# Performance work log

Hardware: AMD Instinct MI355X
Metric: run time of the kernel (lower is better)

The kernel has to match this reference:

```python
import jax, jax.numpy as jnp
import numpy as np

D = 512        # latent_dim
DT = 256       # text_latent_dim
H = 8          # num_heads
TE = 2048      # time_embed_dim
NEG = -1000000.0


def _ln(x, g, b, eps=1e-5):
    m = jnp.mean(x, axis=-1, keepdims=True)
    v = jnp.mean(jnp.square(x - m), axis=-1, keepdims=True)
    return (x - m) * jax.lax.rsqrt(v + eps) * g + b


def _linear(x, W, b):
    return x @ W.T + b


def setup_inputs() -> dict:
    key = jax.random.key(0)
    ks = jax.random.split(key, 24)
    B, T, NT, R, LR = 32, 1024, 77, 4, 256
    inp = {
        'x': jax.random.normal(ks[0], (B, T, D), jnp.float32),
        'xf': jax.random.normal(ks[1], (B, NT, DT), jnp.float32),
        'emb': jax.random.normal(ks[2], (B, TE), jnp.float32),
        'src_mask': jax.random.randint(ks[3], (B, T, 1), 0, 2).astype(jnp.float32),
        'cond_type': jax.random.randint(ks[4], (B, 1, 1), 0, 100).astype(jnp.int32),
        're_motion': jax.random.normal(ks[5], (B, R, LR, D), jnp.float32),
        're_text': jax.random.normal(ks[6], (B, R, 1, D), jnp.float32),
        're_mask': jax.random.randint(ks[7], (B, R, LR), 0, 2).astype(jnp.float32),
    }
    s = 0.02
    def W(k, o, i):
        return jax.random.normal(k, (o, i), jnp.float32) * s
    params = {
        'norm_g': jnp.ones((D,), jnp.float32), 'norm_b': jnp.zeros((D,), jnp.float32),
        'tnorm_g': jnp.ones((DT,), jnp.float32), 'tnorm_b': jnp.zeros((DT,), jnp.float32),
        'rn1_g': jnp.ones((2 * D,), jnp.float32), 'rn1_b': jnp.zeros((2 * D,), jnp.float32),
        'rn2_g': jnp.ones((D,), jnp.float32), 'rn2_b': jnp.zeros((D,), jnp.float32),
        'Wq': W(ks[8], D, D), 'bq': jnp.zeros((D,), jnp.float32),
        'Wkt': W(ks[9], D, DT), 'bkt': jnp.zeros((D,), jnp.float32),
        'Wvt': W(ks[10], D, DT), 'bvt': jnp.zeros((D,), jnp.float32),
        'Wkm': W(ks[11], D, D), 'bkm': jnp.zeros((D,), jnp.float32),
        'Wvm': W(ks[12], D, D), 'bvm': jnp.zeros((D,), jnp.float32),
        'Wkr': W(ks[13], D, 2 * D), 'bkr': jnp.zeros((D,), jnp.float32),
        'Wvr': W(ks[14], D, D), 'bvr': jnp.zeros((D,), jnp.float32),
        'emb_W': W(ks[15], 2 * D, TE), 'emb_b': jnp.zeros((2 * D,), jnp.float32),
        'snorm_g': jnp.ones((D,), jnp.float32), 'snorm_b': jnp.zeros((D,), jnp.float32),
        'out_W': W(ks[16], D, D), 'out_b': jnp.zeros((D,), jnp.float32),
    }
    inp.update(params)
    return inp


def _forward(x, xf, emb, src_mask, cond_type, re_motion, re_text, re_mask,
             norm_g, norm_b, tnorm_g, tnorm_b, rn1_g, rn1_b, rn2_g, rn2_b,
             Wq, bq, Wkt, bkt, Wvt, bvt, Wkm, bkm, Wvm, bvm, Wkr, bkr, Wvr, bvr,
             emb_W, emb_b, snorm_g, snorm_b, out_W, out_b):
    B, T, _ = x.shape
    re_mask_r = re_mask.reshape(B, -1, 1)                       # [B, R*LR, 1]
    N = xf.shape[1] + T + re_motion.shape[1] * re_motion.shape[2]

    xn = _ln(x, norm_g, norm_b)                                  # [B,T,D]
    xfn = _ln(xf, tnorm_g, tnorm_b)                              # [B,NT,DT]
    query = _linear(xn, Wq, bq)                                  # [B,T,D]

    text_ct = (cond_type % 10 > 0).astype(x.dtype)               # [B,1,1]
    retr_ct = (cond_type // 10 > 0).astype(x.dtype)              # [B,1,1]

    re_text_rep = jnp.broadcast_to(re_text, re_motion.shape)     # repeat along Lr
    re_feat_key = jnp.concatenate([re_motion, re_text_rep], axis=-1).reshape(B, -1, 2 * D)

    k_text = _linear(xfn, Wkt, bkt) + (1.0 - text_ct) * NEG
    k_retr = (_linear(_ln(re_feat_key, rn1_g, rn1_b), Wkr, bkr)
              + (1.0 - retr_ct) * NEG + (1.0 - re_mask_r) * NEG)
    k_mot = _linear(xn, Wkm, bkm) + (1.0 - src_mask) * NEG
    key_cat = jnp.concatenate([k_text, k_retr, k_mot], axis=1)   # [B,N,D]

    q = jax.nn.softmax(query.reshape(B, T, H, -1), axis=-1)      # softmax over head_dim
    k = jax.nn.softmax(key_cat.reshape(B, N, H, -1), axis=1)     # softmax over tokens

    re_feat_value = re_motion.reshape(B, -1, D)
    v_text = _linear(xfn, Wvt, bvt) * text_ct
    v_retr = _linear(_ln(re_feat_value, rn2_g, rn2_b), Wvr, bvr) * retr_ct * re_mask_r
    v_mot = _linear(xn, Wvm, bvm) * src_mask
    v = jnp.concatenate([v_text, v_retr, v_mot], axis=1).reshape(B, N, H, -1)

    attention = jnp.einsum('bnhd,bnhl->bhdl', k, v)              # [B,H,hd,hd]
    y = jnp.einsum('bthd,bhdl->bthl', q, attention).reshape(B, T, D)

    # StylizationBlock: film-style scale/shift from time embedding, zero-init out proj
    emb_out = _linear(jax.nn.silu(emb), emb_W, emb_b)[:, None, :]  # [B,1,2D]
    scale, shift = emb_out[..., :D], emb_out[..., D:]
    h = _ln(y, snorm_g, snorm_b) * (1.0 + scale) + shift
    h = _linear(jax.nn.silu(h), out_W, out_b)
    return x + h


def reference(x, xf, emb, src_mask, cond_type, re_motion, re_text, re_mask,
              norm_g, norm_b, tnorm_g, tnorm_b, rn1_g, rn1_b, rn2_g, rn2_b,
              Wq, bq, Wkt, bkt, Wvt, bvt, Wkm, bkm, Wvm, bvm, Wkr, bkr, Wvr, bvr,
              emb_W, emb_b, snorm_g, snorm_b, out_W, out_b):
    return _forward(x, xf, emb, src_mask, cond_type, re_motion, re_text, re_mask,
                    norm_g, norm_b, tnorm_g, tnorm_b, rn1_g, rn1_b, rn2_g, rn2_b,
                    Wq, bq, Wkt, bkt, Wvt, bvt, Wkm, bkm, Wvm, bvm, Wkr, bkr, Wvr, bvr,
                    emb_W, emb_b, snorm_g, snorm_b, out_W, out_b)
```

## Files before the change

kernel.cpp:

```cpp
#include <hip/hip_runtime.h>
#include <cstddef>
#include <cstdint>

#define DEV __device__ __forceinline__

namespace {

constexpr int kH = 8;
constexpr int kB = 32, kT = 1024, kNT = 77, kR = 4, kLR = 256;
constexpr int kRL = kR * kLR;
constexpr float kNEG = -1000000.0f;
constexpr int kNtot = 2304;
constexpr int kNS2 = 3;

typedef __bf16 bf16x8 __attribute__((ext_vector_type(8)));
typedef float f32x4 __attribute__((ext_vector_type(4)));

DEV unsigned short f2bf(float f) {
  unsigned int u = __float_as_uint(f);
  u += 0x7fffu + ((u >> 16) & 1u);
  return (unsigned short)(u >> 16);
}
DEV float bf2f(unsigned short h) { return __uint_as_float(((unsigned int)h) << 16); }

DEV float wave_sum(float v) {
  #pragma unroll
  for (int s = 32; s; s >>= 1) v += __shfl_xor(v, s);
  return v;
}

DEV int xcd_swz(int bid, int nwg) {
  if ((nwg & 7) == 0) return (bid & 7) * (nwg >> 3) + (bid >> 3);
  return bid;
}

template<int COLS>
__global__ __launch_bounds__(256) void ln_bf16(const float* __restrict__ in,
    const float* __restrict__ g, const float* __restrict__ be,
    unsigned short* __restrict__ out) {
  constexpr int PT = COLS / 256;
  int row = blockIdx.x;
  const float* p = in + (size_t)row * COLS;
  unsigned short* o = out + (size_t)row * COLS;
  float v[PT]; float s = 0.f, s2 = 0.f;
  #pragma unroll
  for (int i = 0; i < PT; i++) {
    v[i] = p[threadIdx.x + i * 256];
    s += v[i]; s2 += v[i] * v[i];
  }
  __shared__ float red[2][4];
  int lane = threadIdx.x & 63, w = threadIdx.x >> 6;
  s = wave_sum(s); s2 = wave_sum(s2);
  if (!lane) { red[0][w] = s; red[1][w] = s2; }
  __syncthreads();
  s = red[0][0] + red[0][1] + red[0][2] + red[0][3];
  s2 = red[1][0] + red[1][1] + red[1][2] + red[1][3];
  float mean = s / COLS;
  float var = s2 / COLS - mean * mean;
  float rstd = rsqrtf(var + 1e-5f);
  #pragma unroll
  for (int i = 0; i < PT; i++) {
    int c = threadIdx.x + i * 256;
    o[c] = f2bf((v[i] - mean) * rstd * g[c] + be[c]);
  }
}

__global__ __launch_bounds__(256) void rfk_stats(const float* __restrict__ mot,
    const float* __restrict__ txt, unsigned short* __restrict__ mot_bf,
    float* __restrict__ s1k, float* __restrict__ s2k,
    float* __restrict__ s1v, float* __restrict__ s2v) {
  int m = blockIdx.x;
  const float* pm = mot + (size_t)m * 512;
  const float* pt = txt + (size_t)(m >> 8) * 512;
  float v[2], t[2];
  float sv = 0.f, sv2 = 0.f, st = 0.f, st2 = 0.f;
  #pragma unroll
  for (int i = 0; i < 2; i++) {
    v[i] = pm[threadIdx.x + i * 256]; sv += v[i]; sv2 += v[i] * v[i];
    t[i] = pt[threadIdx.x + i * 256]; st += t[i]; st2 += t[i] * t[i];
  }
  __shared__ float red[4][4];
  int lane = threadIdx.x & 63, w = threadIdx.x >> 6;
  sv = wave_sum(sv); sv2 = wave_sum(sv2); st = wave_sum(st); st2 = wave_sum(st2);
  if (!lane) { red[0][w] = sv; red[1][w] = sv2; red[2][w] = st; red[3][w] = st2; }
  __syncthreads();
  #pragma unroll
  for (int i = 0; i < 2; i++)
    mot_bf[(size_t)m * 512 + threadIdx.x + i * 256] = f2bf(v[i]);
  if (threadIdx.x == 0) {
    float SV = red[0][0] + red[0][1] + red[0][2] + red[0][3];
    float SV2 = red[1][0] + red[1][1] + red[1][2] + red[1][3];
    float ST = red[2][0] + red[2][1] + red[2][2] + red[2][3];
    float ST2 = red[3][0] + red[3][1] + red[3][2] + red[3][3];
    float SA = SV + ST, SA2 = SV2 + ST2;
    float ma = SA / 1024.f, va = SA2 / 1024.f - ma * ma;
    float ra = rsqrtf(va + 1e-5f);
    float mv = SV / 512.f, vv = SV2 / 512.f - mv * mv;
    float rv = rsqrtf(vv + 1e-5f);
    s1k[m] = ra; s2k[m] = -ra * ma;
    s1v[m] = rv; s2v[m] = -rv * mv;
  }
}

__global__ __launch_bounds__(256) void prep_w(
    const float* __restrict__ Wkr, const float* __restrict__ g1,
    const float* __restrict__ b1, const float* __restrict__ bkr,
    const float* __restrict__ Wvr, const float* __restrict__ g2,
    const float* __restrict__ b2, const float* __restrict__ bvr,
    unsigned short* __restrict__ w1lo, unsigned short* __restrict__ w2,
    float* __restrict__ G1, float* __restrict__ B1,
    float* __restrict__ G2, float* __restrict__ B2) {
  int n = blockIdx.x;
  int tid = threadIdx.x;
  float gs = 0.f, bs = 0.f;
  #pragma unroll
  for (int i = 0; i < 4; i++) {
    int k = tid + i * 256;
    float w = Wkr[(size_t)n * 1024 + k];
    float gv = g1[k];
    gs += gv * w; bs += b1[k] * w;
    if (i < 2) w1lo[(size_t)n * 512 + k] = f2bf(gv * w);
  }
  float g2s = 0.f, b2s = 0.f;
  #pragma unroll
  for (int i = 0; i < 2; i++) {
    int k = tid + i * 256;
    float w = Wvr[(size_t)n * 512 + k];
    g2s += g2[k] * w; b2s += b2[k] * w;
    w2[(size_t)n * 512 + k] = f2bf(g2[k] * w);
  }
  __shared__ float red[4][4];
  int lane = tid & 63, w_ = tid >> 6;
  gs = wave_sum(gs); bs = wave_sum(bs); g2s = wave_sum(g2s); b2s = wave_sum(b2s);
  if (!lane) { red[0][w_] = gs; red[1][w_] = bs; red[2][w_] = g2s; red[3][w_] = b2s; }
  __syncthreads();
  if (tid == 0) {
    G1[n] = red[0][0] + red[0][1] + red[0][2] + red[0][3];
    B1[n] = red[1][0] + red[1][1] + red[1][2] + red[1][3] + bkr[n];
    G2[n] = red[2][0] + red[2][1] + red[2][2] + red[2][3];
    B2[n] = red[3][0] + red[3][1] + red[3][2] + red[3][3] + bvr[n];
  }
}

__global__ __launch_bounds__(256) void text_T(const float* __restrict__ re_text,
    const float* __restrict__ g1, const float* __restrict__ Wkr,
    float* __restrict__ T) {
  int m = blockIdx.x;
  int ns = blockIdx.y;
  __shared__ float tr[512];
  int tid = threadIdx.x;
  #pragma unroll
  for (int i = 0; i < 2; i++) {
    int k = tid + i * 256;
    tr[k] = re_text[(size_t)m * 512 + k] * g1[512 + k];
  }
  __syncthreads();
  int n = ns * 64 + (tid >> 2);
  int k0 = (tid & 3) * 128;
  const float* wp = Wkr + (size_t)n * 1024 + 512 + k0;
  float acc = 0.f;
  #pragma unroll
  for (int k = 0; k < 128; k += 4) {
    float4 w4 = *reinterpret_cast<const float4*>(wp + k);
    float4 t4 = *reinterpret_cast<const float4*>(&tr[k0 + k]);
    acc = fmaf(t4.x, w4.x, fmaf(t4.y, w4.y, fmaf(t4.z, w4.z, fmaf(t4.w, w4.w, acc))));
  }
  acc += __shfl_xor(acc, 1);
  acc += __shfl_xor(acc, 2);
  if ((tid & 3) == 0) T[(size_t)m * 512 + n] = acc;
}

__global__ __launch_bounds__(256) void rowmask_kernel(const int* __restrict__ ct,
    const float* __restrict__ src_mask, const float* __restrict__ re_mask,
    float* __restrict__ kaT, float* __restrict__ kaR, float* __restrict__ kaM,
    float* __restrict__ vmT, float* __restrict__ vmR, float* __restrict__ vmM,
    int nB) {
  int i = blockIdx.x * 256 + threadIdx.x;
  if (i < nB * kRL) {
    int b = i >> 10;
    int c = ct[b];
    float retr = (c / 10 > 0) ? 1.f : 0.f;
    float rm = re_mask[i];
    kaR[i] = (1.f - retr) * kNEG + (1.f - rm) * kNEG;
    vmR[i] = retr * rm;
    float sm = src_mask[i];
    kaM[i] = (1.f - sm) * kNEG;
    vmM[i] = sm;
  }
  if (i < nB * kNT) {
    int b = i / kNT;
    int c = ct[b];
    float text = (c % 10 > 0) ? 1.f : 0.f;
    kaT[i] = (1.f - text) * kNEG;
    vmT[i] = text;
  }
}

__global__ __launch_bounds__(256) void castw(const float* __restrict__ s,
    unsigned short* __restrict__ d, int n) {
  int i = (blockIdx.x * 256 + threadIdx.x) * 4;
  if (i < n) {
    float4 v = *reinterpret_cast<const float4*>(s + i);
    ushort4 o;
    o.x = f2bf(v.x); o.y = f2bf(v.y); o.z = f2bf(v.z); o.w = f2bf(v.w);
    *reinterpret_cast<ushort4*>(d + i) = o;
  }
}

__global__ __launch_bounds__(256) void zpad_kernel(unsigned short* __restrict__ E,
    unsigned short* __restrict__ V, int rows) {
  int i = blockIdx.x * 256 + threadIdx.x;
  if (i >= rows * 24) return;
  int row = i / 24, c = i % 24;
  size_t off = (size_t)row * kNtot + 2112 + c * 8;
  ulonglong2 z; z.x = 0; z.y = 0;
  *reinterpret_cast<ulonglong2*>(E + off) = z;
  *reinterpret_cast<ulonglong2*>(V + off) = z;
}

__global__ __launch_bounds__(256) void silu_emb(const float* __restrict__ emb,
    float* __restrict__ semb) {
  int i = (blockIdx.x * 256 + threadIdx.x) * 4;
  float4 v = *reinterpret_cast<const float4*>(emb + i);
  float4 o;
  o.x = v.x / (1.f + __expf(-v.x));
  o.y = v.y / (1.f + __expf(-v.y));
  o.z = v.z / (1.f + __expf(-v.z));
  o.w = v.w / (1.f + __expf(-v.w));
  *reinterpret_cast<float4*>(semb + i) = o;
}

__global__ __launch_bounds__(256) void emb_gemv2(const float* __restrict__ semb,
    const float* __restrict__ W, float* __restrict__ part) {
  int n = blockIdx.x * 4 + (threadIdx.x >> 6);
  int s = blockIdx.y;
  int lane = threadIdx.x & 63;
  int k = s * 256 + lane * 4;
  float4 wv = *reinterpret_cast<const float4*>(&W[(size_t)n * 2048 + k]);
  float acc[32];
  #pragma unroll
  for (int m = 0; m < 32; m++) {
    float4 sv = *reinterpret_cast<const float4*>(&semb[(size_t)m * 2048 + k]);
    acc[m] = fmaf(sv.x, wv.x, fmaf(sv.y, wv.y, fmaf(sv.z, wv.z, sv.w * wv.w)));
  }
  #pragma unroll
  for (int m = 0; m < 32; m++) {
    float t = wave_sum(acc[m]);
    if (lane == 0) part[((size_t)s * 32 + m) * 1024 + n] = t;
  }
}
__global__ __launch_bounds__(256) void emb_fin(const float* __restrict__ part,
    const float* __restrict__ bias, float* __restrict__ ss) {
  int i = blockIdx.x * 256 + threadIdx.x;
  float s = 0.f;
  #pragma unroll
  for (int c = 0; c < 8; c++) s += part[(size_t)c * 32768 + i];
  ss[i] = s + bias[i & 1023];
}

__global__ __launch_bounds__(256) void res_kernel(const unsigned short* __restrict__ c,
    const float* __restrict__ x, float* __restrict__ out, int n4) {
  for (int i = blockIdx.x * 256 + threadIdx.x; i < n4; i += gridDim.x * 256) {
    int j = i * 4;
    ushort4 cv = *reinterpret_cast<const ushort4*>(c + j);
    float4 xv = *reinterpret_cast<const float4*>(x + j);
    float4 o;
    o.x = xv.x + bf2f(cv.x); o.y = xv.y + bf2f(cv.y);
    o.z = xv.z + bf2f(cv.z); o.w = xv.w + bf2f(cv.w);
    *reinterpret_cast<float4*>(out + j) = o;
  }
}

template<int COMBO, int NX>
__global__ __launch_bounds__(256) void gemm_fused(
    const unsigned short* __restrict__ A, const unsigned short* __restrict__ W,
    int M, int K, int m_per_b, int out_off,
    unsigned short* __restrict__ qout,
    unsigned short* __restrict__ E, unsigned short* __restrict__ V,
    const float* __restrict__ biasA, const float* __restrict__ biasB,
    const float* __restrict__ biasC,
    const float* __restrict__ rowAddK, const float* __restrict__ rowMulV,
    const float* __restrict__ s1k, const float* __restrict__ s2k,
    const float* __restrict__ s1v, const float* __restrict__ s2v,
    const float* __restrict__ G1v, const float* __restrict__ G2v,
    const float* __restrict__ Tt) {
  __shared__ __align__(16) char smem[49152];
  unsigned short* lds = (unsigned short*)smem;
  const int tid = threadIdx.x;
  const int lane = tid & 63;
  const int wv = tid >> 6;
  const int wr = (wv >> 1) * 64;
  const int wc = (wv & 1) * 64;
  const int wg = xcd_swz(blockIdx.x, gridDim.x);
  const int m0 = (wg / NX) * 128;
  const int n0 = (wg % NX) * 128;
  const int sec = n0 >> 9;
  const int nlo = n0 & 511;

  const unsigned short* srcA[2]; const unsigned short* srcB[2];
  int dstOff[2];
  #pragma unroll
  for (int i = 0; i < 2; i++) {
    int lin = i * 256 + tid;
    int r = lin >> 2, cl = lin & 3;
    int cs = cl ^ ((r >> 1) & 3);
    int ra = m0 + r; if (ra > M - 1) ra = M - 1;
    srcA[i] = A + (size_t)ra * K + cs * 8;
    srcB[i] = W + (size_t)(n0 + r) * K + cs * 8;
    dstOff[i] = lin * 8;
  }
  int offA[4], offB[4];
  #pragma unroll
  for (int i = 0; i < 4; i++) {
    int r = wr + i * 16 + (lane & 15);
    int c = (lane >> 4) ^ ((r >> 1) & 3);
    offA[i] = r * 32 + c * 8;
    int rb = wc + i * 16 + (lane & 15);
    int cb = (lane >> 4) ^ ((rb >> 1) & 3);
    offB[i] = rb * 32 + cb * 8;
  }

  f32x4 acc[4][4] = {};
  const int nt = K >> 5;

  #pragma unroll
  for (int i = 0; i < 2; i++) {
    __builtin_amdgcn_global_load_lds(
        (const __attribute__((address_space(1))) void*)(srcA[i]),
        (__attribute__((address_space(3))) void*)&lds[dstOff[i]], 16, 0, 0);
    __builtin_amdgcn_global_load_lds(
        (const __attribute__((address_space(1))) void*)(srcB[i]),
        (__attribute__((address_space(3))) void*)&lds[4096 + dstOff[i]], 16, 0, 0);
  }

  int cur = 0;
  for (int t = 0; t < nt; t++) {
    int nxt = cur + 1; if (nxt == 3) nxt = 0;
    if (t + 1 < nt) {
      int ko = (t + 1) << 5;
      #pragma unroll
      for (int i = 0; i < 2; i++) {
        __builtin_amdgcn_global_load_lds(
            (const __attribute__((address_space(1))) void*)(srcA[i] + ko),
            (__attribute__((address_space(3))) void*)&lds[nxt * 8192 + dstOff[i]], 16, 0, 0);
        __builtin_amdgcn_global_load_lds(
            (const __attribute__((address_space(1))) void*)(srcB[i] + ko),
            (__attribute__((address_space(3))) void*)&lds[nxt * 8192 + 4096 + dstOff[i]], 16, 0, 0);
      }
      asm volatile("s_waitcnt vmcnt(4)" ::: "memory");
    } else {
      asm volatile("s_waitcnt vmcnt(0)" ::: "memory");
    }
    __builtin_amdgcn_s_barrier();
    __builtin_amdgcn_sched_barrier(0);
    bf16x8 af[4], bf[4];
    #pragma unroll
    for (int i = 0; i < 4; i++) {
      af[i] = *reinterpret_cast<const bf16x8*>(&lds[cur * 8192 + offA[i]]);
      bf[i] = *reinterpret_cast<const bf16x8*>(&lds[cur * 8192 + 4096 + offB[i]]);
    }
    #pragma unroll
    for (int i = 0; i < 4; i++)
      #pragma unroll
      for (int j = 0; j < 4; j++)
        acc[i][j] = __builtin_amdgcn_mfma_f32_16x16x32_bf16(af[i], bf[j], acc[i][j], 0, 0, 0);
    cur = nxt;
  }
  __syncthreads();

  const int r4 = (lane >> 4) << 2;
  const int rowb = m0 + wr + r4;

  auto epival = [&](float accv, int rowg, int cl) -> float {
    if (COMBO == 0) {
      if (sec == 0) return __expf(accv + biasA[cl]);
      if (sec == 1) return __expf(accv + biasB[cl] + rowAddK[rowg]);
      return (accv + biasC[cl]) * rowMulV[rowg];
    } else if (COMBO == 1) {
      if (sec == 0)
        return __expf((accv + Tt[(size_t)(rowg >> 8) * 512 + cl]) * s1k[rowg]
                      + s2k[rowg] * G1v[cl] + biasA[cl] + rowAddK[rowg]);
      return (accv * s1v[rowg] + s2v[rowg] * G2v[cl] + biasB[cl]) * rowMulV[rowg];
    } else {
      if (sec == 0) return __expf(accv + biasA[cl] + rowAddK[rowg]);
      return (accv + biasB[cl]) * rowMulV[rowg];
    }
  };

  unsigned short* dstEV = (COMBO == 0) ? (sec == 1 ? E : V) : (sec == 0 ? E : V);

  if (COMBO == 2) {
    #pragma unroll
    for (int i = 0; i < 4; i++) {
      #pragma unroll
      for (int r = 0; r < 4; r++) {
        int row = rowb + i * 16 + r;
        if (row >= M) continue;
        size_t nn = out_off + (row % m_per_b);
        size_t cb = (size_t)(row / m_per_b) * 512;
        #pragma unroll
        for (int j = 0; j < 4; j++) {
          int cl = nlo + wc + j * 16 + (lane & 15);
          dstEV[(cb + cl) * kNtot + nn] = f2bf(epival(acc[i][j][r], row, cl));
        }
      }
    }
    return;
  }

  unsigned short* S = (unsigned short*)smem;
  #pragma unroll
  for (int i = 0; i < 4; i++) {
    #pragma unroll
    for (int r = 0; r < 4; r++) {
      int row_t = wr + i * 16 + r4 + r;
      int rowg = m0 + row_t; if (rowg > M - 1) rowg = M - 1;
      int key = ((row_t >> 3) & 7) << 3;
      #pragma unroll
      for (int j = 0; j < 4; j++) {
        int col_t = wc + j * 16 + (lane & 15);
        S[row_t * 128 + (col_t ^ key)] = f2bf(epival(acc[i][j][r], rowg, nlo + col_t));
      }
    }
  }
  __syncthreads();
  bool linear = (COMBO == 0 && sec == 0);
  if (linear) {
    #pragma unroll
    for (int it = 0; it < 8; it++) {
      int slot = it * 256 + tid;
      int row_t = slot >> 4;
      int cs = (slot & 15) * 8;
      int key = ((row_t >> 3) & 7) << 3;
      int row = m0 + row_t;
      if (row < M) {
        ulonglong2 d = *reinterpret_cast<const ulonglong2*>(&S[row_t * 128 + (cs ^ key)]);
        *reinterpret_cast<ulonglong2*>(qout + (size_t)row * 512 + nlo + cs) = d;
      }
    }
  } else {
    #pragma unroll
    for (int it = 0; it < 8; it++) {
      int slot = it * 256 + tid;
      int col_t = slot >> 4;
      int mcx = slot & 15;
      int mc = mcx * 8;
      int key = (mcx & 7) << 3;
      union { unsigned short u[8]; ulonglong2 v; } w;
      #pragma unroll
      for (int e = 0; e < 8; e++)
        w.u[e] = S[(mc + e) * 128 + (col_t ^ key)];
      int row = m0 + mc;
      size_t obase = ((size_t)(row / m_per_b) * 512 + nlo + col_t) * (size_t)kNtot
                   + out_off + (row % m_per_b);
      *reinterpret_cast<ulonglong2*>(dstEV + obase) = w.v;
    }
  }
}

__global__ __launch_bounds__(256) void gemm_mfma(
    const unsigned short* __restrict__ A, const unsigned short* __restrict__ W,
    const float* __restrict__ bias, unsigned short* __restrict__ Cout,
    int M, int K) {
  __shared__ __align__(16) char smem[49152];
  unsigned short* lds = (unsigned short*)smem;
  const int tid = threadIdx.x;
  const int lane = tid & 63;
  const int wv = tid >> 6;
  const int wr = (wv >> 1) * 64;
  const int wc = (wv & 1) * 64;
  const int wg = xcd_swz(blockIdx.x, gridDim.x);
  const int m0 = (wg >> 2) * 128;
  const int n0 = (wg & 3) * 128;

  const unsigned short* srcA[2]; const unsigned short* srcB[2];
  int dstOff[2];
  #pragma unroll
  for (int i = 0; i < 2; i++) {
    int lin = i * 256 + tid;
    int r = lin >> 2, cl = lin & 3;
    int cs = cl ^ ((r >> 1) & 3);
    int ra = m0 + r; if (ra > M - 1) ra = M - 1;
    srcA[i] = A + (size_t)ra * K + cs * 8;
    srcB[i] = W + (size_t)(n0 + r) * K + cs * 8;
    dstOff[i] = lin * 8;
  }
  int offA[4], offB[4];
  #pragma unroll
  for (int i = 0; i < 4; i++) {
    int r = wr + i * 16 + (lane & 15);
    int c = (lane >> 4) ^ ((r >> 1) & 3);
    offA[i] = r * 32 + c * 8;
    int rb = wc + i * 16 + (lane & 15);
    int cb = (lane >> 4) ^ ((rb >> 1) & 3);
    offB[i] = rb * 32 + cb * 8;
  }

  f32x4 acc[4][4] = {};
  const int nt = K >> 5;

  #pragma unroll
  for (int i = 0; i < 2; i++) {
    __builtin_amdgcn_global_load_lds(
        (const __attribute__((address_space(1))) void*)(srcA[i]),
        (__attribute__((address_space(3))) void*)&lds[dstOff[i]], 16, 0, 0);
    __builtin_amdgcn_global_load_lds(
        (const __attribute__((address_space(1))) void*)(srcB[i]),
        (__attribute__((address_space(3))) void*)&lds[4096 + dstOff[i]], 16, 0, 0);
  }

  int cur = 0;
  for (int t = 0; t < nt; t++) {
    int nxt = cur + 1; if (nxt == 3) nxt = 0;
    if (t + 1 < nt) {
      int ko = (t + 1) << 5;
      #pragma unroll
      for (int i = 0; i < 2; i++) {
        __builtin_amdgcn_global_load_lds(
            (const __attribute__((address_space(1))) void*)(srcA[i] + ko),
            (__attribute__((address_space(3))) void*)&lds[nxt * 8192 + dstOff[i]], 16, 0, 0);
        __builtin_amdgcn_global_load_lds(
            (const __attribute__((address_space(1))) void*)(srcB[i] + ko),
            (__attribute__((address_space(3))) void*)&lds[nxt * 8192 + 4096 + dstOff[i]], 16, 0, 0);
      }
      asm volatile("s_waitcnt vmcnt(4)" ::: "memory");
    } else {
      asm volatile("s_waitcnt vmcnt(0)" ::: "memory");
    }
    __builtin_amdgcn_s_barrier();
    __builtin_amdgcn_sched_barrier(0);
    bf16x8 af[4], bf[4];
    #pragma unroll
    for (int i = 0; i < 4; i++) {
      af[i] = *reinterpret_cast<const bf16x8*>(&lds[cur * 8192 + offA[i]]);
      bf[i] = *reinterpret_cast<const bf16x8*>(&lds[cur * 8192 + 4096 + offB[i]]);
    }
    #pragma unroll
    for (int i = 0; i < 4; i++)
      #pragma unroll
      for (int j = 0; j < 4; j++)
        acc[i][j] = __builtin_amdgcn_mfma_f32_16x16x32_bf16(af[i], bf[j], acc[i][j], 0, 0, 0);
    cur = nxt;
  }
  __syncthreads();

  const int r4 = (lane >> 4) << 2;
  unsigned short* S = (unsigned short*)smem;
  #pragma unroll
  for (int i = 0; i < 4; i++) {
    #pragma unroll
    for (int r = 0; r < 4; r++) {
      int row_t = wr + i * 16 + r4 + r;
      int key = ((row_t >> 3) & 7) << 3;
      #pragma unroll
      for (int j = 0; j < 4; j++) {
        int col_t = wc + j * 16 + (lane & 15);
        S[row_t * 128 + (col_t ^ key)] = f2bf(acc[i][j][r] + bias[n0 + col_t]);
      }
    }
  }
  __syncthreads();
  #pragma unroll
  for (int it = 0; it < 8; it++) {
    int slot = it * 256 + tid;
    int row_t = slot >> 4;
    int cs = (slot & 15) * 8;
    int key = ((row_t >> 3) & 7) << 3;
    int row = m0 + row_t;
    if (row < M) {
      ulonglong2 d = *reinterpret_cast<const ulonglong2*>(&S[row_t * 128 + (cs ^ key)]);
      *reinterpret_cast<ulonglong2*>(Cout + (size_t)row * 512 + n0 + cs) = d;
    }
  }
}

__global__ __launch_bounds__(256) void attp_kernel(const unsigned short* __restrict__ E,
    const unsigned short* __restrict__ V, float* __restrict__ part,
    float* __restrict__ part_cs) {
  int bh = blockIdx.x;
  int s = blockIdx.y;
  const unsigned short* Ep = E + (size_t)bh * 64 * kNtot;
  const unsigned short* Vp = V + (size_t)bh * 64 * kNtot;
  __shared__ __align__(16) char smem[34816];
  unsigned short* Elds = (unsigned short*)smem;
  unsigned short* Vlds = (unsigned short*)(smem + 17408);
  int tid = threadIdx.x, lane = tid & 63, wv = tid >> 6;
  f32x4 acc[4] = {};
  float csum = 0.f;
  int cd = tid & 63, cq = tid >> 6;
  const int arow = (wv * 16 + (lane & 15)) * 136 + ((lane >> 4) << 3);
  const int brow0 = ((lane & 15)) * 136 + ((lane >> 4) << 3);

  for (int it = 0; it < 6; it++) {
    int n0 = s * 768 + it * 128;
    __syncthreads();
    #pragma unroll
    for (int r = 0; r < 4; r++) {
      int ch = r * 256 + tid;
      int d = ch >> 4, off = (ch & 15) * 8;
      *reinterpret_cast<ulonglong2*>(&Elds[d * 136 + off]) =
          *reinterpret_cast<const ulonglong2*>(Ep + (size_t)d * kNtot + n0 + off);
      *reinterpret_cast<ulonglong2*>(&Vlds[d * 136 + off]) =
          *reinterpret_cast<const ulonglong2*>(Vp + (size_t)d * kNtot + n0 + off);
    }
    __syncthreads();
    #pragma unroll
    for (int ks = 0; ks < 4; ks++) {
      bf16x8 af = *reinterpret_cast<const bf16x8*>(&Elds[arow + ks * 32]);
      #pragma unroll
      for (int j = 0; j < 4; j++) {
        bf16x8 bf = *reinterpret_cast<const bf16x8*>(&Vlds[brow0 + j * 16 * 136 + ks * 32]);
        acc[j] = __builtin_amdgcn_mfma_f32_16x16x32_bf16(af, bf, acc[j], 0, 0, 0);
      }
    }
    #pragma unroll
    for (int k8 = 0; k8 < 4; k8++) {
      bf16x8 ev = *reinterpret_cast<const bf16x8*>(&Elds[cd * 136 + cq * 32 + k8 * 8]);
      const unsigned short* pu = reinterpret_cast<const unsigned short*>(&ev);
      #pragma unroll
      for (int e = 0; e < 8; e++) csum += bf2f(pu[e]);
    }
  }
  float* op = part + ((size_t)bh * kNS2 + s) * 4096;
  int dbase = wv * 16 + ((lane >> 4) << 2);
  #pragma unroll
  for (int j = 0; j < 4; j++)
    #pragma unroll
    for (int r = 0; r < 4; r++)
      op[(dbase + r) * 64 + j * 16 + (lane & 15)] = acc[j][r];
  __syncthreads();
  float* csu = (float*)smem;
  csu[cq * 64 + cd] = csum;
  __syncthreads();
  if (tid < 64)
    part_cs[((size_t)bh * kNS2 + s) * 64 + tid] =
        csu[tid] + csu[64 + tid] + csu[128 + tid] + csu[192 + tid];
}

__global__ __launch_bounds__(256) void attc_kernel(const float* __restrict__ part,
    const float* __restrict__ part_cs, unsigned short* __restrict__ attT) {
  int bh = blockIdx.x;
  __shared__ float at[64][65];
  __shared__ float sinv[64];
  int tid = threadIdx.x;
  if (tid < 64) {
    float s = 0.f;
    #pragma unroll
    for (int c = 0; c < kNS2; c++) s += part_cs[((size_t)bh * kNS2 + c) * 64 + tid];
    sinv[tid] = 1.f / s;
  }
  for (int i = tid; i < 4096; i += 256) {
    float s = 0.f;
    #pragma unroll
    for (int c = 0; c < kNS2; c++) s += part[((size_t)bh * kNS2 + c) * 4096 + i];
    at[i >> 6][i & 63] = s;
  }
  __syncthreads();
  for (int j = tid; j < 4096; j += 256) {
    int l = j >> 6, d = j & 63;
    attT[(size_t)bh * 4096 + j] = f2bf(at[d][l] * sinv[d]);
  }
}

__global__ __launch_bounds__(256) void y_mfma(const unsigned short* __restrict__ q,
    const unsigned short* __restrict__ attT, unsigned short* __restrict__ y) {
  int bh = blockIdx.x; int b = bh >> 3, h = bh & 7;
  int t0 = blockIdx.y * 128;
  __shared__ unsigned short bt[64][72];
  __shared__ float rs[128];
  __shared__ unsigned short ob[128][72];
  int tid = threadIdx.x, lane = tid & 63, wv = tid >> 6;
  int wr = wv * 32;
  for (int i = tid; i < 512; i += 256) {
    int row = i >> 3, c8 = (i & 7) * 8;
    *reinterpret_cast<ulonglong2*>(&bt[row][c8]) =
        *reinterpret_cast<const ulonglong2*>(attT + (size_t)bh * 4096 + row * 64 + c8);
  }
  const unsigned short* qp = q + ((size_t)(b * 1024 + t0 + wr)) * 512 + h * 64;
  bf16x8 af[2][2];
  #pragma unroll
  for (int i = 0; i < 2; i++) {
    int row = i * 16 + (lane & 15);
    #pragma unroll
    for (int s = 0; s < 2; s++)
      af[i][s] = *reinterpret_cast<const bf16x8*>(qp + (size_t)row * 512 + s * 32 + (lane >> 4) * 8);
  }
  #pragma unroll
  for (int i = 0; i < 2; i++) {
    float r = 0.f;
    #pragma unroll
    for (int s = 0; s < 2; s++) {
      const unsigned short* pu = reinterpret_cast<const unsigned short*>(&af[i][s]);
      #pragma unroll
      for (int e = 0; e < 8; e++) r += bf2f(pu[e]);
    }
    r += __shfl_xor(r, 16); r += __shfl_xor(r, 32);
    if (lane < 16) rs[wr + i * 16 + lane] = r;
  }
  __syncthreads();
  f32x4 acc[2][4] = {};
  #pragma unroll
  for (int s = 0; s < 2; s++) {
    #pragma unroll
    for (int j = 0; j < 4; j++) {
      bf16x8 bf = *reinterpret_cast<const bf16x8*>(&bt[j * 16 + (lane & 15)][s * 32 + (lane >> 4) * 8]);
      #pragma unroll
      for (int i = 0; i < 2; i++)
        acc[i][j] = __builtin_amdgcn_mfma_f32_16x16x32_bf16(af[i][s], bf, acc[i][j], 0, 0, 0);
    }
  }
  int r4 = (lane >> 4) << 2;
  #pragma unroll
  for (int i = 0; i < 2; i++) {
    #pragma unroll
    for (int r = 0; r < 4; r++) {
      int row = wr + i * 16 + r4 + r;
      float rinv = 1.f / rs[row];
      #pragma unroll
      for (int j = 0; j < 4; j++)
        ob[row][j * 16 + (lane & 15)] = f2bf(acc[i][j][r] * rinv);
    }
  }
  __syncthreads();
  for (int i = tid; i < 1024; i += 256) {
    int row = i >> 3, c8 = (i & 7) * 8;
    *reinterpret_cast<ulonglong2*>(y + ((size_t)(b * 1024 + t0 + row)) * 512 + h * 64 + c8) =
        *reinterpret_cast<const ulonglong2*>(&ob[row][c8]);
  }
}

__global__ __launch_bounds__(256) void mod_kernel(const unsigned short* __restrict__ y,
    const float* __restrict__ ss, const float* __restrict__ g, const float* __restrict__ be,
    unsigned short* __restrict__ h) {
  int row = blockIdx.x; int b = row >> 10;
  const unsigned short* p = y + (size_t)row * 512;
  unsigned short* o = h + (size_t)row * 512;
  float v[2]; float s = 0.f, s2 = 0.f;
  #pragma unroll
  for (int i = 0; i < 2; i++) {
    v[i] = bf2f(p[threadIdx.x + i * 256]);
    s += v[i]; s2 += v[i] * v[i];
  }
  __shared__ float red[2][4];
  int lane = threadIdx.x & 63, w = threadIdx.x >> 6;
  s = wave_sum(s); s2 = wave_sum(s2);
  if (!lane) { red[0][w] = s; red[1][w] = s2; }
  __syncthreads();
  s = red[0][0] + red[0][1] + red[0][2] + red[0][3];
  s2 = red[1][0] + red[1][1] + red[1][2] + red[1][3];
  float mean = s / 512.f, var = s2 / 512.f - mean * mean;
  float rstd = rsqrtf(var + 1e-5f);
  #pragma unroll
  for (int i = 0; i < 2; i++) {
    int c = threadIdx.x + i * 256;
    float val = (v[i] - mean) * rstd * g[c] + be[c];
    val = val * (1.f + ss[b * 1024 + c]) + ss[b * 1024 + 512 + c];
    o[c] = f2bf(val / (1.f + __expf(-val)));
  }
}

}

extern "C" void kernel_launch(void* const* d_in, const int* in_sizes, int n_in,
                              void* d_out, int out_size, void* d_ws, size_t ws_size,
                              hipStream_t stream) {
  const float* x        = (const float*)d_in[0];
  const float* xf       = (const float*)d_in[1];
  const float* emb      = (const float*)d_in[2];
  const float* src_mask = (const float*)d_in[3];
  const int*   cond     = (const int*)d_in[4];
  const float* re_motion= (const float*)d_in[5];
  const float* re_text  = (const float*)d_in[6];
  const float* re_mask  = (const float*)d_in[7];
  const float* norm_g = (const float*)d_in[8],  * norm_b = (const float*)d_in[9];
  const float* tnorm_g= (const float*)d_in[10], * tnorm_b= (const float*)d_in[11];
  const float* rn1_g  = (const float*)d_in[12], * rn1_b  = (const float*)d_in[13];
  const float* rn2_g  = (const float*)d_in[14], * rn2_b  = (const float*)d_in[15];
  const float* Wq  = (const float*)d_in[16], * bq  = (const float*)d_in[17];
  const float* Wkt = (const float*)d_in[18], * bkt = (const float*)d_in[19];
  const float* Wvt = (const float*)d_in[20], * bvt = (const float*)d_in[21];
  const float* Wkm = (const float*)d_in[22], * bkm = (const float*)d_in[23];
  const float* Wvm = (const float*)d_in[24], * bvm = (const float*)d_in[25];
  const float* Wkr = (const float*)d_in[26], * bkr = (const float*)d_in[27];
  const float* Wvr = (const float*)d_in[28], * bvr = (const float*)d_in[29];
  const float* emb_W = (const float*)d_in[30], * emb_b = (const float*)d_in[31];
  const float* snorm_g = (const float*)d_in[32], * snorm_b = (const float*)d_in[33];
  const float* out_W = (const float*)d_in[34], * out_b = (const float*)d_in[35];
  float* out = (float*)d_out;

  char* base = (char*)d_ws;
  size_t off = 0;
  auto ab = [&](size_t nb) { char* p = base + off; off = (off + nb + 255) & ~(size_t)255; return p; };

  unsigned short* wcat0 = (unsigned short*)ab((size_t)1536 * 512 * 2);
  unsigned short* wcat1 = (unsigned short*)ab((size_t)1024 * 512 * 2);
  unsigned short* wcat2 = (unsigned short*)ab((size_t)1024 * 256 * 2);
  unsigned short* wout_bf= (unsigned short*)ab(512 * 512 * 2);
  float* G1 = (float*)ab(512 * 4); float* B1 = (float*)ab(512 * 4);
  float* G2 = (float*)ab(512 * 4); float* B2 = (float*)ab(512 * 4);
  float* Tbuf = (float*)ab((size_t)kB * kR * 512 * 4);
  float* semb_f   = (float*)ab((size_t)kB * 2048 * 4);
  float* part_emb = (float*)ab((size_t)8 * kB * 1024 * 4);
  float* ssb_full = (float*)ab((size_t)kB * 1024 * 4);
  float* kaT_full = (float*)ab((size_t)kB * kNT * 4);
  float* vmT_full = (float*)ab((size_t)kB * kNT * 4);
  float* kaR_full = (float*)ab((size_t)kB * kRL * 4);
  float* kaM_full = (float*)ab((size_t)kB * kT * 4);
  float* vmR_full = (float*)ab((size_t)kB * kRL * 4);
  float* vmM_full = (float*)ab((size_t)kB * kT * 4);
  const size_t fixed_off = off;

  auto pad = [](size_t n) { return (n + 255) & ~(size_t)255; };
  auto att_bytes = [&](size_t CH) -> size_t {
    return pad(CH * 8 * 4096 * 2)
         + pad(CH * 8 * (size_t)kNS2 * 4096 * 4)
         + pad(CH * 8 * (size_t)kNS2 * 64 * 4);
  };
  auto chunk_bytes = [&](size_t CH) -> size_t {
    size_t xnr = pad(CH * 1024 * 512 * 2);
    if (att_bytes(CH) > xnr) xnr = att_bytes(CH);
    size_t s = 0;
    s += xnr;
    s += pad(CH * kNT * 256 * 2);
    s += pad(CH * 1024 * 512 * 2);
    s += 4 * pad(CH * 1024 * 4);
    s += pad(CH * 1024 * 512 * 2);
    s += pad((size_t)CH * 512 * kNtot * 2);
    s += pad((size_t)CH * 512 * kNtot * 2);
    return s;
  };
  int CH = 32;
  while (CH > 1 && fixed_off + chunk_bytes(CH) > ws_size) CH >>= 1;

  auto cl = [&](const float* s, unsigned short* d, int n) {
    castw<<<dim3((n / 4 + 255) / 256), 256, 0, stream>>>(s, d, n);
  };
  cl(Wq,  wcat0,              512 * 512);
  cl(Wkm, wcat0 + 512 * 512,  512 * 512);
  cl(Wvm, wcat0 + 1024 * 512, 512 * 512);
  cl(Wkt, wcat2,              512 * 256);
  cl(Wvt, wcat2 + 512 * 256,  512 * 256);
  cl(out_W, wout_bf, 512 * 512);
  prep_w<<<dim3(512), 256, 0, stream>>>(Wkr, rn1_g, rn1_b, bkr, Wvr, rn2_g, rn2_b, bvr,
                                        wcat1, wcat1 + 512 * 512, G1, B1, G2, B2);
  text_T<<<dim3(kB * kR, 8), 256, 0, stream>>>(re_text, rn1_g, Wkr, Tbuf);

  rowmask_kernel<<<dim3(kB * 4), 256, 0, stream>>>(cond, src_mask, re_mask,
      kaT_full, kaR_full, kaM_full, vmT_full, vmR_full, vmM_full, kB);
  silu_emb<<<dim3(kB * 2048 / 1024), 256, 0, stream>>>(emb, semb_f);
  emb_gemv2<<<dim3(256, 8), 256, 0, stream>>>(semb_f, emb_W, part_emb);
  emb_fin<<<dim3(128), 256, 0, stream>>>(part_emb, emb_b, ssb_full);

  for (int b0 = 0; b0 < kB; b0 += CH) {
    off = fixed_off;
    const int MRc = CH * 1024;
    const int MTc = CH * kNT;

    size_t xnr = pad((size_t)MRc * 512 * 2);
    if (att_bytes(CH) > xnr) xnr = att_bytes(CH);
    char* xnR = ab(xnr);
    unsigned short* xn_bf  = (unsigned short*)xnR;
    unsigned short* attT = (unsigned short*)xnR;
    float* attp = (float*)(xnR + pad((size_t)CH * 8 * 4096 * 2));
    float* part_cs = (float*)(xnR + pad((size_t)CH * 8 * 4096 * 2)
                                  + pad((size_t)CH * 8 * (size_t)kNS2 * 4096 * 4));
    unsigned short* h_bf = xn_bf;

    unsigned short* xfn_bf = (unsigned short*)ab((size_t)MTc * 256 * 2);
    unsigned short* mot_bf = (unsigned short*)ab((size_t)MRc * 512 * 2);
    float* s1k = (float*)ab((size_t)CH * 1024 * 4);
    float* s2k = (float*)ab((size_t)CH * 1024 * 4);
    float* s1v = (float*)ab((size_t)CH * 1024 * 4);
    float* s2v = (float*)ab((size_t)CH * 1024 * 4);
    unsigned short* qb_bf  = (unsigned short*)ab((size_t)MRc * 512 * 2);
    unsigned short* kc_bf  = (unsigned short*)ab((size_t)CH * 512 * kNtot * 2);
    unsigned short* vb_bf  = (unsigned short*)ab((size_t)CH * 512 * kNtot * 2);
    unsigned short* yb16 = mot_bf;
    unsigned short* cfin = qb_bf;

    const float* x_c   = x + (size_t)b0 * kT * 512;
    const float* xf_c  = xf + (size_t)b0 * kNT * 256;
    const float* rm_c  = re_motion + (size_t)b0 * kRL * 512;
    const float* rt_c  = re_text + (size_t)b0 * kR * 512;
    float* out_c = out + (size_t)b0 * kT * 512;

    ln_bf16<512><<<dim3(MRc), 256, 0, stream>>>(x_c, norm_g, norm_b, xn_bf);
    ln_bf16<256><<<dim3(MTc), 256, 0, stream>>>(xf_c, tnorm_g, tnorm_b, xfn_bf);
    rfk_stats<<<dim3(MRc), 256, 0, stream>>>(rm_c, rt_c, mot_bf, s1k, s2k, s1v, s2v);
    zpad_kernel<<<dim3(CH * 48), 256, 0, stream>>>(kc_bf, vb_bf, CH * 512);

    gemm_fused<0, 12><<<dim3(12 * CH * 8), 256, 0, stream>>>(
        xn_bf, wcat0, MRc, 512, kT, kNT + kRL,
        qb_bf, kc_bf, vb_bf, bq, bkm, bvm,
        kaM_full + (size_t)b0 * kT, vmM_full + (size_t)b0 * kT,
        nullptr, nullptr, nullptr, nullptr, nullptr, nullptr, nullptr);
    gemm_fused<1, 8><<<dim3(8 * CH * 8), 256, 0, stream>>>(
        mot_bf, wcat1, MRc, 512, kRL, kNT,
        nullptr, kc_bf, vb_bf, B1, B2, nullptr,
        kaR_full + (size_t)b0 * kRL, vmR_full + (size_t)b0 * kRL,
        s1k, s2k, s1v, s2v, G1, G2, Tbuf + (size_t)b0 * kR * 512);
    gemm_fused<2, 8><<<dim3(8 * ((MTc + 127) / 128)), 256, 0, stream>>>(
        xfn_bf, wcat2, MTc, 256, kNT, 0,
        nullptr, kc_bf, vb_bf, bkt, bvt, nullptr,
        kaT_full + (size_t)b0 * kNT, vmT_full + (size_t)b0 * kNT,
        nullptr, nullptr, nullptr, nullptr, nullptr, nullptr, nullptr);

    attp_kernel<<<dim3(CH * 8, kNS2), 256, 0, stream>>>(kc_bf, vb_bf, attp, part_cs);
    attc_kernel<<<dim3(CH * 8), 256, 0, stream>>>(attp, part_cs, attT);
    y_mfma<<<dim3(CH * 8, 8), 256, 0, stream>>>(qb_bf, attT, yb16);

    mod_kernel<<<dim3(MRc), 256, 0, stream>>>(yb16, ssb_full + (size_t)b0 * 1024,
                                              snorm_g, snorm_b, h_bf);
    gemm_mfma<<<dim3(4 * CH * 8), 256, 0, stream>>>(h_bf, wout_bf, out_b, cfin, MRc, 512);
    res_kernel<<<dim3(2048), 256, 0, stream>>>(cfin, x_c, out_c, MRc * 128);
  }
}
```

Baseline: 509.6 us.

## Fuse residual add into output GEMM and merge attention split-K kernels

The residual add moves into the output GEMM epilogue, which reads x and writes the fp32 output directly, so the bf16 intermediate round trip and the separate residual kernel go away. The attention k^T v kernel stops splitting the sequence across three blocks per (batch, head). Each block now loops over all 18 tiles and normalizes and transposes its result in LDS, which removes the attc kernel and the partial buffers. The cost is less parallelism in attp (CH*8 blocks instead of CH*24), so the longer serial loop per block may underuse the GPU.

```diff
diff --git a/kernel.cpp b/kernel.cpp
--- a/kernel.cpp
+++ b/kernel.cpp
@@ -11,7 +11,6 @@
 constexpr int kRL = kR * kLR;
 constexpr float kNEG = -1000000.0f;
 constexpr int kNtot = 2304;
-constexpr int kNS2 = 3;
 
 typedef __bf16 bf16x8 __attribute__((ext_vector_type(8)));
 typedef float f32x4 __attribute__((ext_vector_type(4)));
@@ -256,19 +255,6 @@
   #pragma unroll
   for (int c = 0; c < 8; c++) s += part[(size_t)c * 32768 + i];
   ss[i] = s + bias[i & 1023];
-}
-
-__global__ __launch_bounds__(256) void res_kernel(const unsigned short* __restrict__ c,
-    const float* __restrict__ x, float* __restrict__ out, int n4) {
-  for (int i = blockIdx.x * 256 + threadIdx.x; i < n4; i += gridDim.x * 256) {
-    int j = i * 4;
-    ushort4 cv = *reinterpret_cast<const ushort4*>(c + j);
-    float4 xv = *reinterpret_cast<const float4*>(x + j);
-    float4 o;
-    o.x = xv.x + bf2f(cv.x); o.y = xv.y + bf2f(cv.y);
-    o.z = xv.z + bf2f(cv.z); o.w = xv.w + bf2f(cv.w);
-    *reinterpret_cast<float4*>(out + j) = o;
-  }
 }
 
 template<int COMBO, int NX>
@@ -460,8 +446,8 @@
 
 __global__ __launch_bounds__(256) void gemm_mfma(
     const unsigned short* __restrict__ A, const unsigned short* __restrict__ W,
-    const float* __restrict__ bias, unsigned short* __restrict__ Cout,
-    int M, int K) {
+    const float* __restrict__ bias, const float* __restrict__ Xres,
+    float* __restrict__ Outf, int M, int K) {
   __shared__ __align__(16) char smem[49152];
   unsigned short* lds = (unsigned short*)smem;
   const int tid = threadIdx.x;
@@ -568,17 +554,26 @@
     int key = ((row_t >> 3) & 7) << 3;
     int row = m0 + row_t;
     if (row < M) {
-      ulonglong2 d = *reinterpret_cast<const ulonglong2*>(&S[row_t * 128 + (cs ^ key)]);
-      *reinterpret_cast<ulonglong2*>(Cout + (size_t)row * 512 + n0 + cs) = d;
+      union { unsigned short u[8]; ulonglong2 v; } w;
+      w.v = *reinterpret_cast<const ulonglong2*>(&S[row_t * 128 + (cs ^ key)]);
+      const float* xp = Xres + (size_t)row * 512 + n0 + cs;
+      float4 x0 = *reinterpret_cast<const float4*>(xp);
+      float4 x1 = *reinterpret_cast<const float4*>(xp + 4);
+      float4 o0, o1;
+      o0.x = x0.x + bf2f(w.u[0]); o0.y = x0.y + bf2f(w.u[1]);
+      o0.z = x0.z + bf2f(w.u[2]); o0.w = x0.w + bf2f(w.u[3]);
+      o1.x = x1.x + bf2f(w.u[4]); o1.y = x1.y + bf2f(w.u[5]);
+      o1.z = x1.z + bf2f(w.u[6]); o1.w = x1.w + bf2f(w.u[7]);
+      float* op = Outf + (size_t)row * 512 + n0 + cs;
+      *reinterpret_cast<float4*>(op) = o0;
+      *reinterpret_cast<float4*>(op + 4) = o1;
     }
   }
 }
 
 __global__ __launch_bounds__(256) void attp_kernel(const unsigned short* __restrict__ E,
-    const unsigned short* __restrict__ V, float* __restrict__ part,
-    float* __restrict__ part_cs) {
+    const unsigned short* __restrict__ V, unsigned short* __restrict__ attT) {
   int bh = blockIdx.x;
-  int s = blockIdx.y;
   const unsigned short* Ep = E + (size_t)bh * 64 * kNtot;
   const unsigned short* Vp = V + (size_t)bh * 64 * kNtot;
   __shared__ __align__(16) char smem[34816];
@@ -591,8 +586,8 @@
   const int arow = (wv * 16 + (lane & 15)) * 136 + ((lane >> 4) << 3);
   const int brow0 = ((lane & 15)) * 136 + ((lane >> 4) << 3);
 
-  for (int it = 0; it < 6; it++) {
-    int n0 = s * 768 + it * 128;
+  for (int it = 0; it < 18; it++) {
+    int n0 = it * 128;
     __syncthreads();
     #pragma unroll
     for (int r = 0; r < 4; r++) {
@@ -621,44 +616,26 @@
       for (int e = 0; e < 8; e++) csum += bf2f(pu[e]);
     }
   }
-  float* op = part + ((size_t)bh * kNS2 + s) * 4096;
+  __syncthreads();
+  float* atf = (float*)(smem + 17408);
+  float* csu = (float*)smem;
+  float* sinv = (float*)(smem + 1024);
   int dbase = wv * 16 + ((lane >> 4) << 2);
   #pragma unroll
   for (int j = 0; j < 4; j++)
     #pragma unroll
     for (int r = 0; r < 4; r++)
-      op[(dbase + r) * 64 + j * 16 + (lane & 15)] = acc[j][r];
-  __syncthreads();
-  float* csu = (float*)smem;
+      atf[(dbase + r) * 65 + j * 16 + (lane & 15)] = acc[j][r];
   csu[cq * 64 + cd] = csum;
   __syncthreads();
-  if (tid < 64)
-    part_cs[((size_t)bh * kNS2 + s) * 64 + tid] =
-        csu[tid] + csu[64 + tid] + csu[128 + tid] + csu[192 + tid];
-}
-
-__global__ __launch_bounds__(256) void attc_kernel(const float* __restrict__ part,
-    const float* __restrict__ part_cs, unsigned short* __restrict__ attT) {
-  int bh = blockIdx.x;
-  __shared__ float at[64][65];
-  __shared__ float sinv[64];
-  int tid = threadIdx.x;
   if (tid < 64) {
-    float s = 0.f;
-    #pragma unroll
-    for (int c = 0; c < kNS2; c++) s += part_cs[((size_t)bh * kNS2 + c) * 64 + tid];
+    float s = csu[tid] + csu[64 + tid] + csu[128 + tid] + csu[192 + tid];
     sinv[tid] = 1.f / s;
-  }
-  for (int i = tid; i < 4096; i += 256) {
-    float s = 0.f;
-    #pragma unroll
-    for (int c = 0; c < kNS2; c++) s += part[((size_t)bh * kNS2 + c) * 4096 + i];
-    at[i >> 6][i & 63] = s;
   }
   __syncthreads();
   for (int j = tid; j < 4096; j += 256) {
     int l = j >> 6, d = j & 63;
-    attT[(size_t)bh * 4096 + j] = f2bf(at[d][l] * sinv[d]);
+    attT[(size_t)bh * 4096 + j] = f2bf(atf[d * 65 + l] * sinv[d]);
   }
 }
 
@@ -811,16 +788,9 @@
   const size_t fixed_off = off;
 
   auto pad = [](size_t n) { return (n + 255) & ~(size_t)255; };
-  auto att_bytes = [&](size_t CH) -> size_t {
-    return pad(CH * 8 * 4096 * 2)
-         + pad(CH * 8 * (size_t)kNS2 * 4096 * 4)
-         + pad(CH * 8 * (size_t)kNS2 * 64 * 4);
-  };
   auto chunk_bytes = [&](size_t CH) -> size_t {
-    size_t xnr = pad(CH * 1024 * 512 * 2);
-    if (att_bytes(CH) > xnr) xnr = att_bytes(CH);
     size_t s = 0;
-    s += xnr;
+    s += pad(CH * 1024 * 512 * 2);
     s += pad(CH * kNT * 256 * 2);
     s += pad(CH * 1024 * 512 * 2);
     s += 4 * pad(CH * 1024 * 4);
@@ -856,15 +826,10 @@
     const int MRc = CH * 1024;
     const int MTc = CH * kNT;
 
-    size_t xnr = pad((size_t)MRc * 512 * 2);
-    if (att_bytes(CH) > xnr) xnr = att_bytes(CH);
-    char* xnR = ab(xnr);
+    char* xnR = ab(pad((size_t)MRc * 512 * 2));
     unsigned short* xn_bf  = (unsigned short*)xnR;
     unsigned short* attT = (unsigned short*)xnR;
-    float* attp = (float*)(xnR + pad((size_t)CH * 8 * 4096 * 2));
-    float* part_cs = (float*)(xnR + pad((size_t)CH * 8 * 4096 * 2)
-                                  + pad((size_t)CH * 8 * (size_t)kNS2 * 4096 * 4));
-    unsigned short* h_bf = xn_bf;
+    unsigned short* h_bf = (unsigned short*)xnR;
 
     unsigned short* xfn_bf = (unsigned short*)ab((size_t)MTc * 256 * 2);
     unsigned short* mot_bf = (unsigned short*)ab((size_t)MRc * 512 * 2);
@@ -876,7 +841,6 @@
     unsigned short* kc_bf  = (unsigned short*)ab((size_t)CH * 512 * kNtot * 2);
     unsigned short* vb_bf  = (unsigned short*)ab((size_t)CH * 512 * kNtot * 2);
     unsigned short* yb16 = mot_bf;
-    unsigned short* cfin = qb_bf;
 
     const float* x_c   = x + (size_t)b0 * kT * 512;
     const float* xf_c  = xf + (size_t)b0 * kNT * 256;
@@ -905,13 +869,12 @@
         kaT_full + (size_t)b0 * kNT, vmT_full + (size_t)b0 * kNT,
         nullptr, nullptr, nullptr, nullptr, nullptr, nullptr, nullptr);
 
-    attp_kernel<<<dim3(CH * 8, kNS2), 256, 0, stream>>>(kc_bf, vb_bf, attp, part_cs);
-    attc_kernel<<<dim3(CH * 8), 256, 0, stream>>>(attp, part_cs, attT);
+    attp_kernel<<<dim3(CH * 8), 256, 0, stream>>>(kc_bf, vb_bf, attT);
     y_mfma<<<dim3(CH * 8, 8), 256, 0, stream>>>(qb_bf, attT, yb16);
 
     mod_kernel<<<dim3(MRc), 256, 0, stream>>>(yb16, ssb_full + (size_t)b0 * 1024,
                                               snorm_g, snorm_b, h_bf);
-    gemm_mfma<<<dim3(4 * CH * 8), 256, 0, stream>>>(h_bf, wout_bf, out_b, cfin, MRc, 512);
-    res_kernel<<<dim3(2048), 256, 0, stream>>>(cfin, x_c, out_c, MRc * 128);
-  }
-}
+    gemm_mfma<<<dim3(4 * CH * 8), 256, 0, stream>>>(h_bf, wout_bf, out_b,
+                                                    x_c, out_c, MRc, 512);
+  }
+}
```

Result: slower. 531.8 us (+4.3%).
